# Optimization experiments

Hardware: AMD Instinct MI355X
Metric: run time of the kernel (lower is better)

The kernel has to match this reference:

```python
import jax, jax.numpy as jnp
import numpy as np

IN_F = 4096
OUT_F = 4096
BITS = 8
EPS = 1e-5
BATCH, SEQ = 4, 2048


def setup_inputs() -> dict:
    key = jax.random.key(0)
    k1, k2, k3 = jax.random.split(key, 3)
    bound = 1.0 / np.sqrt(IN_F)
    x = jax.random.normal(k1, (BATCH, SEQ, IN_F), dtype=jnp.float32)
    weight = jax.random.uniform(k2, (OUT_F, IN_F), dtype=jnp.float32, minval=-bound, maxval=bound)
    bias = jax.random.uniform(k3, (OUT_F,), dtype=jnp.float32, minval=-bound, maxval=bound)
    return {"x": x, "weight": weight, "bias": bias}


def _ste_round_clip(v, lo, hi):
    # round+clip with straight-through estimator
    q = jnp.clip(jnp.round(v), lo, hi)
    return v + jax.lax.stop_gradient(q - v)


def reference(x, weight, bias):
    q = jnp.float32(2 ** (BITS - 1))  # 128 for int8
    # weight ternarization: absmean scale, round to {-1,0,1}
    w_scale = jnp.maximum(jnp.mean(jnp.abs(weight)), EPS)
    w_q = _ste_round_clip(weight / w_scale, -1.0, 1.0)  # ternary [O,I]
    # activation int8 quantization: absmax scale over whole tensor (dim=None)
    gamma = jnp.maximum(jnp.max(jnp.abs(x)), EPS)
    x_q = _ste_round_clip(x * (q / gamma), -q, q - 1.0)  # int8 range values
    # integer-domain matmul then dequantize
    out = jnp.einsum('bsi,oi->bso', x_q, w_q) * (gamma * w_scale / q)
    return out + bias
```

## Files before the change

### kernel.cpp

```cpp
#include <hip/hip_runtime.h>
#include <stdint.h>

#define GLOBAL_AS __attribute__((address_space(1)))
#define LDS_AS __attribute__((address_space(3)))

typedef int v4i  __attribute__((ext_vector_type(4)));
typedef int v16i __attribute__((ext_vector_type(16)));

static constexpr int M = 8192;
static constexpr int N = 4096;
static constexpr int K = 4096;
static constexpr float F_EPS = 1e-5f;


__global__ void reduce_kernel(const float4* __restrict__ x, const float4* __restrict__ w,
                              float* __restrict__ pmax, double* __restrict__ psum) {
    const int b = blockIdx.x;
    const int t = threadIdx.x;
    if (b < 2048) {
        float m = 0.f;
        const int n4 = M * K / 4;
        int i = b * 512 + t;
        for (; i + 256 < n4; i += 2048 * 512) {
            float4 v0 = x[i];
            float4 v1 = x[i + 256];
            m = fmaxf(m, fmaxf(fmaxf(fabsf(v0.x), fabsf(v0.y)), fmaxf(fabsf(v0.z), fabsf(v0.w))));
            m = fmaxf(m, fmaxf(fmaxf(fabsf(v1.x), fabsf(v1.y)), fmaxf(fabsf(v1.z), fabsf(v1.w))));
        }
#pragma unroll
        for (int off = 32; off > 0; off >>= 1) m = fmaxf(m, __shfl_down(m, off, 64));
        __shared__ float red[4];
        if ((t & 63) == 0) red[t >> 6] = m;
        __syncthreads();
        if (t == 0) pmax[b] = fmaxf(fmaxf(red[0], red[1]), fmaxf(red[2], red[3]));
    } else {
        double s = 0.0;
        const int n4 = N * K / 4;
        int i = (b - 2048) * 512 + t;
        for (; i + 256 < n4; i += 1024 * 512) {
            float4 v0 = w[i];
            float4 v1 = w[i + 256];
            s += (double)fabsf(v0.x) + (double)fabsf(v0.y) + (double)fabsf(v0.z) + (double)fabsf(v0.w);
            s += (double)fabsf(v1.x) + (double)fabsf(v1.y) + (double)fabsf(v1.z) + (double)fabsf(v1.w);
        }
#pragma unroll
        for (int off = 32; off > 0; off >>= 1) s += __shfl_down(s, off, 64);
        __shared__ double dred[4];
        if ((t & 63) == 0) dred[t >> 6] = s;
        __syncthreads();
        if (t == 0) psum[b - 2048] = dred[0] + dred[1] + dred[2] + dred[3];
    }
}

__global__ void finalize_kernel(float* __restrict__ wssc, const float* __restrict__ pmax,
                                const double* __restrict__ psum) {
    const int t = threadIdx.x;
    float m = 0.f;
#pragma unroll
    for (int j = 0; j < 8; ++j) m = fmaxf(m, pmax[t + j * 256]);
#pragma unroll
    for (int off = 32; off > 0; off >>= 1) m = fmaxf(m, __shfl_down(m, off, 64));
    double s = psum[t] + psum[t + 256] + psum[t + 512] + psum[t + 768];
#pragma unroll
    for (int off = 32; off > 0; off >>= 1) s += __shfl_down(s, off, 64);
    __shared__ float red[4];
    __shared__ double dred[4];
    if ((t & 63) == 0) { red[t >> 6] = m; dred[t >> 6] = s; }
    __syncthreads();
    if (t == 0) {
        float gamma = fmaxf(fmaxf(fmaxf(red[0], red[1]), fmaxf(red[2], red[3])), F_EPS);
        double sum = dred[0] + dred[1] + dred[2] + dred[3];
        float wscale = (float)fmax(sum * (1.0 / ((double)N * (double)K)), (double)F_EPS);
        wssc[0] = 128.f / gamma;
        wssc[1] = wscale;
        wssc[2] = gamma * wscale / 128.f;
    }
}

__global__ void quant_kernel(const float4* __restrict__ x, const float4* __restrict__ w,
                             int* __restrict__ xq, int* __restrict__ wq,
                             const float* __restrict__ wssc) {
    const int b = blockIdx.x;
    const int t = threadIdx.x;
    if (b < 2048) {
        const float s = wssc[0];
        const int n4 = M * K / 4;
        int i = b * 512 + t;
        for (; i + 256 < n4; i += 2048 * 512) {
            float4 v0 = x[i];
            float4 v1 = x[i + 256];
            int a0 = min(127, max(-128, (int)rintf(v0.x * s)));
            int a1 = min(127, max(-128, (int)rintf(v0.y * s)));
            int a2 = min(127, max(-128, (int)rintf(v0.z * s)));
            int a3 = min(127, max(-128, (int)rintf(v0.w * s)));
            xq[i] = (a0 & 255) | ((a1 & 255) << 8) | ((a2 & 255) << 16) | (a3 << 24);
            int b0 = min(127, max(-128, (int)rintf(v1.x * s)));
            int b1 = min(127, max(-128, (int)rintf(v1.y * s)));
            int b2 = min(127, max(-128, (int)rintf(v1.z * s)));
            int b3 = min(127, max(-128, (int)rintf(v1.w * s)));
            xq[i + 256] = (b0 & 255) | ((b1 & 255) << 8) | ((b2 & 255) << 16) | (b3 << 24);
        }
    } else {
        const float ws = wssc[1];
        const int n4 = N * K / 4;
        int i = (b - 2048) * 512 + t;
        for (; i + 256 < n4; i += 1024 * 512) {
            float4 v0 = w[i];
            float4 v1 = w[i + 256];
            int a0 = min(1, max(-1, (int)rintf(v0.x / ws)));
            int a1 = min(1, max(-1, (int)rintf(v0.y / ws)));
            int a2 = min(1, max(-1, (int)rintf(v0.z / ws)));
            int a3 = min(1, max(-1, (int)rintf(v0.w / ws)));
            wq[i] = (a0 & 255) | ((a1 & 255) << 8) | ((a2 & 255) << 16) | (a3 << 24);
            int b0 = min(1, max(-1, (int)rintf(v1.x / ws)));
            int b1 = min(1, max(-1, (int)rintf(v1.y / ws)));
            int b2 = min(1, max(-1, (int)rintf(v1.z / ws)));
            int b3 = min(1, max(-1, (int)rintf(v1.w / ws)));
            wq[i + 256] = (b0 & 255) | ((b1 & 255) << 8) | ((b2 & 255) << 16) | (b3 << 24);
        }
    }
}

__global__ __launch_bounds__(512, 2) void gemm_kernel(
    const int8_t* __restrict__ xq, const int8_t* __restrict__ wq,
    const float* __restrict__ bias, const float* __restrict__ wssc,
    float* __restrict__ out) {

    __shared__ __align__(16) int8_t As[4][256 * 64];
    __shared__ __align__(16) int8_t Bs[4][256 * 64];

    const int t = threadIdx.x;
    const int lane = t & 63;
    const int wv = t >> 6;
    const int half = lane >> 5;
    const int lr = lane & 31;
    const int wm0 = (wv >> 2) * 128;
    const int wn0 = (wv & 3) * 64;

    const int bid = blockIdx.x;
    const int xcd = bid & 7;
    const int cix = bid >> 3;
    const int m0 = ((xcd >> 1) * 8 + (cix >> 3)) * 256;
    const int n0 = ((xcd & 1) * 8 + (cix & 7)) * 256;

    const GLOBAL_AS int8_t* aSrc[2];
    const GLOBAL_AS int8_t* bSrc[2];
    int aLds[2], bLds[2];
#pragma unroll
    for (int j = 0; j < 2; ++j) {
        int idx = j * 512 + t;
        int c = idx >> 6;
        int s = idx & 63;
        int k = s >> 4;
        int rho = ((s & 15) - 4 * k) & 15;
        int row = c * 16 + rho;
        aSrc[j] = (const GLOBAL_AS int8_t*)(xq + (size_t)(m0 + row) * K + k * 16);
        bSrc[j] = (const GLOBAL_AS int8_t*)(wq + (size_t)(n0 + row) * K + k * 16);
        aLds[j] = idx * 16;
        bLds[j] = idx * 16;
    }

    int aOff[2][4], bOff[2][2];
#pragma unroll
    for (int ks = 0; ks < 2; ++ks) {
        int k = ks * 2 + half;
#pragma unroll
        for (int q = 0; q < 4; ++q) {
            int r = wm0 + q * 32 + lr;
            aOff[ks][q] = (r >> 4) * 1024 + k * 256 + (((r & 15) + 4 * k) & 15) * 16;
        }
#pragma unroll
        for (int q = 0; q < 2; ++q) {
            int r = wn0 + q * 32 + lr;
            bOff[ks][q] = (r >> 4) * 1024 + k * 256 + (((r & 15) + 4 * k) & 15) * 16;
        }
    }

    v16i acc[4][2];
#pragma unroll
    for (int mt = 0; mt < 4; ++mt)
#pragma unroll
        for (int nt = 0; nt < 2; ++nt)
#pragma unroll
            for (int e = 0; e < 16; ++e) acc[mt][nt][e] = 0;

    auto stage = [&](int kt, int8_t* A, int8_t* B) {
#pragma unroll
        for (int j = 0; j < 2; ++j)
            __builtin_amdgcn_global_load_lds((const GLOBAL_AS void*)(aSrc[j] + kt),
                                             (LDS_AS void*)(A + aLds[j]), 16, 0, 0);
#pragma unroll
        for (int j = 0; j < 2; ++j)
            __builtin_amdgcn_global_load_lds((const GLOBAL_AS void*)(bSrc[j] + kt),
                                             (LDS_AS void*)(B + bLds[j]), 16, 0, 0);
    };

    auto compute = [&](const int8_t* A, const int8_t* B) {
#pragma unroll
        for (int ks = 0; ks < 2; ++ks) {
            v4i a[4], b[2];
#pragma unroll
            for (int q = 0; q < 4; ++q) a[q] = *(const v4i*)(A + aOff[ks][q]);
#pragma unroll
            for (int q = 0; q < 2; ++q) b[q] = *(const v4i*)(B + bOff[ks][q]);
            __builtin_amdgcn_s_setprio(1);
#pragma unroll
            for (int mt = 0; mt < 4; ++mt)
#pragma unroll
                for (int nt = 0; nt < 2; ++nt)
                    acc[mt][nt] = __builtin_amdgcn_mfma_i32_32x32x32_i8(a[mt], b[nt], acc[mt][nt], 0, 0, 0);
            __builtin_amdgcn_s_setprio(0);
        }
    };

#define FENCE() asm volatile("" ::: "memory")
#define PIPE_STEP(NB, CB, KT)                                        \
    do {                                                             \
        stage((KT) * 64, As[NB], Bs[NB]);                            \
        asm volatile("s_waitcnt vmcnt(12)" ::: "memory");            \
        __builtin_amdgcn_s_barrier();                                \
        FENCE();                                                     \
        compute(As[CB], Bs[CB]);                                     \
        FENCE();                                                     \
        __builtin_amdgcn_s_barrier();                                \
        FENCE();                                                     \
    } while (0)

    stage(0, As[0], Bs[0]);
    stage(64, As[1], Bs[1]);
    stage(128, As[2], Bs[2]);

#pragma unroll 1
    for (int tb = 0; tb < 56; tb += 4) {
        PIPE_STEP(3, 0, tb + 3);
        PIPE_STEP(0, 1, tb + 4);
        PIPE_STEP(1, 2, tb + 5);
        PIPE_STEP(2, 3, tb + 6);
    }
    PIPE_STEP(3, 0, 59);
    PIPE_STEP(0, 1, 60);
    PIPE_STEP(1, 2, 61);
    PIPE_STEP(2, 3, 62);
    PIPE_STEP(3, 0, 63);
    asm volatile("s_waitcnt vmcnt(8)" ::: "memory");
    __builtin_amdgcn_s_barrier(); FENCE();
    compute(As[1], Bs[1]); FENCE();
    __builtin_amdgcn_s_barrier(); FENCE();
    asm volatile("s_waitcnt vmcnt(4)" ::: "memory");
    __builtin_amdgcn_s_barrier(); FENCE();
    compute(As[2], Bs[2]); FENCE();
    __builtin_amdgcn_s_barrier(); FENCE();
    asm volatile("s_waitcnt vmcnt(0)" ::: "memory");
    __builtin_amdgcn_s_barrier(); FENCE();
    compute(As[3], Bs[3]);
#undef PIPE_STEP
#undef FENCE

    const float scale = wssc[2];
#pragma unroll
    for (int nt = 0; nt < 2; ++nt) {
        int col = n0 + wn0 + nt * 32 + lr;
        float bv = bias[col];
#pragma unroll
        for (int mt = 0; mt < 4; ++mt) {
            int rb = m0 + wm0 + mt * 32 + 4 * half;
#pragma unroll
            for (int reg = 0; reg < 16; ++reg) {
                int row = rb + (reg & 3) + 8 * (reg >> 2);
                out[(size_t)row * N + col] = (float)acc[mt][nt][reg] * scale + bv;
            }
        }
    }
}

extern "C" void kernel_launch(void* const* d_in, const int* in_sizes, int n_in,
                              void* d_out, int out_size, void* d_ws, size_t ws_size,
                              hipStream_t stream) {
    const float* x = (const float*)d_in[0];
    const float* w = (const float*)d_in[1];
    const float* bias = (const float*)d_in[2];
    float* out = (float*)d_out;

    float* wssc = (float*)d_ws;
    float* pmax = (float*)((char*)d_ws + 256);
    double* psum = (double*)((char*)d_ws + 8448);
    int8_t* xq = (int8_t*)d_ws + 16640;
    int8_t* wq = xq + (size_t)M * K;

    hipLaunchKernelGGL(reduce_kernel, dim3(3072), dim3(256), 0, stream,
                       (const float4*)x, (const float4*)w, pmax, psum);
    hipLaunchKernelGGL(finalize_kernel, dim3(1), dim3(256), 0, stream, wssc, pmax, psum);
    hipLaunchKernelGGL(quant_kernel, dim3(3072), dim3(256), 0, stream,
                       (const float4*)x, (const float4*)w, (int*)xq, (int*)wq, wssc);
    hipLaunchKernelGGL(gemm_kernel, dim3(M / 128 / 2 * N / 256 / 2 * 2), dim3(512), 0, stream,
                       xq, wq, bias, wssc, out);
}
```

Measured before the change: 459.7 us.

## Interleave staged A/B global loads with per-k-substep MFMA phases in int8 GEMM

Measured after the change: 497.8 us. +8.3%, slower.

```diff
diff --git a/kernel.cpp b/kernel.cpp
--- a/kernel.cpp
+++ b/kernel.cpp
@@ -184,77 +184,78 @@
 #pragma unroll
             for (int e = 0; e < 16; ++e) acc[mt][nt][e] = 0;
 
-    auto stage = [&](int kt, int8_t* A, int8_t* B) {
+    auto stageA = [&](int8_t* A, int kt) {
 #pragma unroll
         for (int j = 0; j < 2; ++j)
             __builtin_amdgcn_global_load_lds((const GLOBAL_AS void*)(aSrc[j] + kt),
                                              (LDS_AS void*)(A + aLds[j]), 16, 0, 0);
+    };
+    auto stageB = [&](int8_t* B, int kt) {
 #pragma unroll
         for (int j = 0; j < 2; ++j)
             __builtin_amdgcn_global_load_lds((const GLOBAL_AS void*)(bSrc[j] + kt),
                                              (LDS_AS void*)(B + bLds[j]), 16, 0, 0);
     };
 
-    auto compute = [&](const int8_t* A, const int8_t* B) {
-#pragma unroll
-        for (int ks = 0; ks < 2; ++ks) {
-            v4i a[4], b[2];
-#pragma unroll
-            for (int q = 0; q < 4; ++q) a[q] = *(const v4i*)(A + aOff[ks][q]);
-#pragma unroll
-            for (int q = 0; q < 2; ++q) b[q] = *(const v4i*)(B + bOff[ks][q]);
-            __builtin_amdgcn_s_setprio(1);
-#pragma unroll
-            for (int mt = 0; mt < 4; ++mt)
-#pragma unroll
-                for (int nt = 0; nt < 2; ++nt)
-                    acc[mt][nt] = __builtin_amdgcn_mfma_i32_32x32x32_i8(a[mt], b[nt], acc[mt][nt], 0, 0, 0);
-            __builtin_amdgcn_s_setprio(0);
-        }
-    };
-
-#define FENCE() asm volatile("" ::: "memory")
-#define PIPE_STEP(NB, CB, KT)                                        \
-    do {                                                             \
-        stage((KT) * 64, As[NB], Bs[NB]);                            \
-        asm volatile("s_waitcnt vmcnt(12)" ::: "memory");            \
-        __builtin_amdgcn_s_barrier();                                \
-        FENCE();                                                     \
-        compute(As[CB], Bs[CB]);                                     \
-        FENCE();                                                     \
-        __builtin_amdgcn_s_barrier();                                \
-        FENCE();                                                     \
+#define MFMA_I8(A_, B_, C_) __builtin_amdgcn_mfma_i32_32x32x32_i8(A_, B_, C_, 0, 0, 0)
+
+#define PHASE(Ab, Bb, KS, STAGEFN)                                          \
+    do {                                                                    \
+        v4i a0_ = *(const v4i*)((Ab) + aOff[KS][0]);                        \
+        v4i a1_ = *(const v4i*)((Ab) + aOff[KS][1]);                        \
+        v4i a2_ = *(const v4i*)((Ab) + aOff[KS][2]);                        \
+        v4i a3_ = *(const v4i*)((Ab) + aOff[KS][3]);                        \
+        v4i b0_ = *(const v4i*)((Bb) + bOff[KS][0]);                        \
+        v4i b1_ = *(const v4i*)((Bb) + bOff[KS][1]);                        \
+        STAGEFN;                                                            \
+        asm volatile("" ::: "memory");                                      \
+        __builtin_amdgcn_s_barrier();                                       \
+        __builtin_amdgcn_s_setprio(1);                                      \
+        acc[0][0] = MFMA_I8(a0_, b0_, acc[0][0]);                           \
+        acc[0][1] = MFMA_I8(a0_, b1_, acc[0][1]);                           \
+        acc[1][0] = MFMA_I8(a1_, b0_, acc[1][0]);                           \
+        acc[1][1] = MFMA_I8(a1_, b1_, acc[1][1]);                           \
+        acc[2][0] = MFMA_I8(a2_, b0_, acc[2][0]);                           \
+        acc[2][1] = MFMA_I8(a2_, b1_, acc[2][1]);                           \
+        acc[3][0] = MFMA_I8(a3_, b0_, acc[3][0]);                           \
+        acc[3][1] = MFMA_I8(a3_, b1_, acc[3][1]);                           \
+        __builtin_amdgcn_s_setprio(0);                                      \
+        asm volatile("" ::: "memory");                                      \
     } while (0)
 
-    stage(0, As[0], Bs[0]);
-    stage(64, As[1], Bs[1]);
-    stage(128, As[2], Bs[2]);
+#define TILE_END(VM)                                                        \
+    do {                                                                    \
+        asm volatile("s_waitcnt vmcnt(" #VM ")" ::: "memory");              \
+        __builtin_amdgcn_s_barrier();                                       \
+    } while (0)
+
+    stageA(As[0], 0);   stageB(Bs[0], 0);
+    stageA(As[1], 64);  stageB(Bs[1], 64);
+    stageA(As[2], 128); stageB(Bs[2], 128);
+    TILE_END(8);
 
 #pragma unroll 1
-    for (int tb = 0; tb < 56; tb += 4) {
-        PIPE_STEP(3, 0, tb + 3);
-        PIPE_STEP(0, 1, tb + 4);
-        PIPE_STEP(1, 2, tb + 5);
-        PIPE_STEP(2, 3, tb + 6);
-    }
-    PIPE_STEP(3, 0, 59);
-    PIPE_STEP(0, 1, 60);
-    PIPE_STEP(1, 2, 61);
-    PIPE_STEP(2, 3, 62);
-    PIPE_STEP(3, 0, 63);
-    asm volatile("s_waitcnt vmcnt(8)" ::: "memory");
-    __builtin_amdgcn_s_barrier(); FENCE();
-    compute(As[1], Bs[1]); FENCE();
-    __builtin_amdgcn_s_barrier(); FENCE();
-    asm volatile("s_waitcnt vmcnt(4)" ::: "memory");
-    __builtin_amdgcn_s_barrier(); FENCE();
-    compute(As[2], Bs[2]); FENCE();
-    __builtin_amdgcn_s_barrier(); FENCE();
-    asm volatile("s_waitcnt vmcnt(0)" ::: "memory");
-    __builtin_amdgcn_s_barrier(); FENCE();
-    compute(As[3], Bs[3]);
-#undef PIPE_STEP
-#undef FENCE
+    for (int tt = 0; tt < 61; ++tt) {
+        const int8_t* Ab = As[tt & 3];
+        const int8_t* Bb = Bs[tt & 3];
+        int8_t* An = As[(tt + 3) & 3];
+        int8_t* Bn = Bs[(tt + 3) & 3];
+        const int kt = (tt + 3) * 64;
+        PHASE(Ab, Bb, 0, stageA(An, kt));
+        PHASE(Ab, Bb, 1, stageB(Bn, kt));
+        TILE_END(8);
+    }
+    PHASE(As[61 & 3], Bs[61 & 3], 0, ((void)0));
+    PHASE(As[61 & 3], Bs[61 & 3], 1, ((void)0));
+    TILE_END(4);
+    PHASE(As[62 & 3], Bs[62 & 3], 0, ((void)0));
+    PHASE(As[62 & 3], Bs[62 & 3], 1, ((void)0));
+    TILE_END(0);
+    PHASE(As[63 & 3], Bs[63 & 3], 0, ((void)0));
+    PHASE(As[63 & 3], Bs[63 & 3], 1, ((void)0));
+#undef PHASE
+#undef TILE_END
+#undef MFMA_I8
 
     const float scale = wssc[2];
 #pragma unroll
@@ -292,6 +293,6 @@
     hipLaunchKernelGGL(finalize_kernel, dim3(1), dim3(256), 0, stream, wssc, pmax, psum);
     hipLaunchKernelGGL(quant_kernel, dim3(3072), dim3(256), 0, stream,
                        (const float4*)x, (const float4*)w, (int*)xq, (int*)wq, wssc);
-    hipLaunchKernelGGL(gemm_kernel, dim3(M / 128 / 2 * N / 256 / 2 * 2), dim3(512), 0, stream,
+    hipLaunchKernelGGL(gemm_kernel, dim3((M / 256) * (N / 256)), dim3(512), 0, stream,
                        xq, wq, bias, wssc, out);
 }
```

## Use 1024-thread blocks with smaller per-wave tiles and a double-buffered loop

Applied to the files above, without the earlier changes.

After: 487.8 us. 6.1% more time.

```diff
diff --git a/kernel.cpp b/kernel.cpp
--- a/kernel.cpp
+++ b/kernel.cpp
@@ -121,20 +121,20 @@
     }
 }
 
-__global__ __launch_bounds__(512, 2) void gemm_kernel(
+__global__ __launch_bounds__(1024, 3) void gemm_kernel(
     const int8_t* __restrict__ xq, const int8_t* __restrict__ wq,
     const float* __restrict__ bias, const float* __restrict__ wssc,
     float* __restrict__ out) {
 
-    __shared__ __align__(16) int8_t As[4][256 * 64];
-    __shared__ __align__(16) int8_t Bs[4][256 * 64];
+    __shared__ __align__(16) int8_t As[2][256 * 64];
+    __shared__ __align__(16) int8_t Bs[2][256 * 64];
 
     const int t = threadIdx.x;
     const int lane = t & 63;
     const int wv = t >> 6;
     const int half = lane >> 5;
     const int lr = lane & 31;
-    const int wm0 = (wv >> 2) * 128;
+    const int wm0 = (wv >> 2) * 64;
     const int wn0 = (wv & 3) * 64;
 
     const int bid = blockIdx.x;
@@ -143,69 +143,61 @@
     const int m0 = ((xcd >> 1) * 8 + (cix >> 3)) * 256;
     const int n0 = ((xcd & 1) * 8 + (cix & 7)) * 256;
 
-    const GLOBAL_AS int8_t* aSrc[2];
-    const GLOBAL_AS int8_t* bSrc[2];
-    int aLds[2], bLds[2];
-#pragma unroll
-    for (int j = 0; j < 2; ++j) {
-        int idx = j * 512 + t;
+    const GLOBAL_AS int8_t* aSrc;
+    const GLOBAL_AS int8_t* bSrc;
+    int ldsOff;
+    {
+        int idx = t;
         int c = idx >> 6;
         int s = idx & 63;
         int k = s >> 4;
         int rho = ((s & 15) - 4 * k) & 15;
         int row = c * 16 + rho;
-        aSrc[j] = (const GLOBAL_AS int8_t*)(xq + (size_t)(m0 + row) * K + k * 16);
-        bSrc[j] = (const GLOBAL_AS int8_t*)(wq + (size_t)(n0 + row) * K + k * 16);
-        aLds[j] = idx * 16;
-        bLds[j] = idx * 16;
-    }
-
-    int aOff[2][4], bOff[2][2];
+        aSrc = (const GLOBAL_AS int8_t*)(xq + (size_t)(m0 + row) * K + k * 16);
+        bSrc = (const GLOBAL_AS int8_t*)(wq + (size_t)(n0 + row) * K + k * 16);
+        ldsOff = idx * 16;
+    }
+
+    int aOff[2][2], bOff[2][2];
 #pragma unroll
     for (int ks = 0; ks < 2; ++ks) {
         int k = ks * 2 + half;
 #pragma unroll
-        for (int q = 0; q < 4; ++q) {
-            int r = wm0 + q * 32 + lr;
-            aOff[ks][q] = (r >> 4) * 1024 + k * 256 + (((r & 15) + 4 * k) & 15) * 16;
-        }
-#pragma unroll
         for (int q = 0; q < 2; ++q) {
-            int r = wn0 + q * 32 + lr;
-            bOff[ks][q] = (r >> 4) * 1024 + k * 256 + (((r & 15) + 4 * k) & 15) * 16;
-        }
-    }
-
-    v16i acc[4][2];
-#pragma unroll
-    for (int mt = 0; mt < 4; ++mt)
+            int ra = wm0 + q * 32 + lr;
+            aOff[ks][q] = (ra >> 4) * 1024 + k * 256 + (((ra & 15) + 4 * k) & 15) * 16;
+            int rb = wn0 + q * 32 + lr;
+            bOff[ks][q] = (rb >> 4) * 1024 + k * 256 + (((rb & 15) + 4 * k) & 15) * 16;
+        }
+    }
+
+    v16i acc[2][2];
+#pragma unroll
+    for (int mt = 0; mt < 2; ++mt)
 #pragma unroll
         for (int nt = 0; nt < 2; ++nt)
 #pragma unroll
             for (int e = 0; e < 16; ++e) acc[mt][nt][e] = 0;
 
     auto stage = [&](int kt, int8_t* A, int8_t* B) {
-#pragma unroll
-        for (int j = 0; j < 2; ++j)
-            __builtin_amdgcn_global_load_lds((const GLOBAL_AS void*)(aSrc[j] + kt),
-                                             (LDS_AS void*)(A + aLds[j]), 16, 0, 0);
-#pragma unroll
-        for (int j = 0; j < 2; ++j)
-            __builtin_amdgcn_global_load_lds((const GLOBAL_AS void*)(bSrc[j] + kt),
-                                             (LDS_AS void*)(B + bLds[j]), 16, 0, 0);
+        __builtin_amdgcn_global_load_lds((const GLOBAL_AS void*)(aSrc + kt),
+                                         (LDS_AS void*)(A + ldsOff), 16, 0, 0);
+        __builtin_amdgcn_global_load_lds((const GLOBAL_AS void*)(bSrc + kt),
+                                         (LDS_AS void*)(B + ldsOff), 16, 0, 0);
     };
 
     auto compute = [&](const int8_t* A, const int8_t* B) {
 #pragma unroll
         for (int ks = 0; ks < 2; ++ks) {
-            v4i a[4], b[2];
-#pragma unroll
-            for (int q = 0; q < 4; ++q) a[q] = *(const v4i*)(A + aOff[ks][q]);
-#pragma unroll
-            for (int q = 0; q < 2; ++q) b[q] = *(const v4i*)(B + bOff[ks][q]);
+            v4i a[2], b[2];
+#pragma unroll
+            for (int q = 0; q < 2; ++q) {
+                a[q] = *(const v4i*)(A + aOff[ks][q]);
+                b[q] = *(const v4i*)(B + bOff[ks][q]);
+            }
             __builtin_amdgcn_s_setprio(1);
 #pragma unroll
-            for (int mt = 0; mt < 4; ++mt)
+            for (int mt = 0; mt < 2; ++mt)
 #pragma unroll
                 for (int nt = 0; nt < 2; ++nt)
                     acc[mt][nt] = __builtin_amdgcn_mfma_i32_32x32x32_i8(a[mt], b[nt], acc[mt][nt], 0, 0, 0);
@@ -213,48 +205,16 @@
         }
     };
 
-#define FENCE() asm volatile("" ::: "memory")
-#define PIPE_STEP(NB, CB, KT)                                        \
-    do {                                                             \
-        stage((KT) * 64, As[NB], Bs[NB]);                            \
-        asm volatile("s_waitcnt vmcnt(12)" ::: "memory");            \
-        __builtin_amdgcn_s_barrier();                                \
-        FENCE();                                                     \
-        compute(As[CB], Bs[CB]);                                     \
-        FENCE();                                                     \
-        __builtin_amdgcn_s_barrier();                                \
-        FENCE();                                                     \
-    } while (0)
-
+    constexpr int NIT = K / 64;
     stage(0, As[0], Bs[0]);
-    stage(64, As[1], Bs[1]);
-    stage(128, As[2], Bs[2]);
-
+    __syncthreads();
 #pragma unroll 1
-    for (int tb = 0; tb < 56; tb += 4) {
-        PIPE_STEP(3, 0, tb + 3);
-        PIPE_STEP(0, 1, tb + 4);
-        PIPE_STEP(1, 2, tb + 5);
-        PIPE_STEP(2, 3, tb + 6);
-    }
-    PIPE_STEP(3, 0, 59);
-    PIPE_STEP(0, 1, 60);
-    PIPE_STEP(1, 2, 61);
-    PIPE_STEP(2, 3, 62);
-    PIPE_STEP(3, 0, 63);
-    asm volatile("s_waitcnt vmcnt(8)" ::: "memory");
-    __builtin_amdgcn_s_barrier(); FENCE();
-    compute(As[1], Bs[1]); FENCE();
-    __builtin_amdgcn_s_barrier(); FENCE();
-    asm volatile("s_waitcnt vmcnt(4)" ::: "memory");
-    __builtin_amdgcn_s_barrier(); FENCE();
-    compute(As[2], Bs[2]); FENCE();
-    __builtin_amdgcn_s_barrier(); FENCE();
-    asm volatile("s_waitcnt vmcnt(0)" ::: "memory");
-    __builtin_amdgcn_s_barrier(); FENCE();
-    compute(As[3], Bs[3]);
-#undef PIPE_STEP
-#undef FENCE
+    for (int tt = 0; tt < NIT - 1; ++tt) {
+        stage((tt + 1) * 64, As[(tt + 1) & 1], Bs[(tt + 1) & 1]);
+        compute(As[tt & 1], Bs[tt & 1]);
+        __syncthreads();
+    }
+    compute(As[(NIT - 1) & 1], Bs[(NIT - 1) & 1]);
 
     const float scale = wssc[2];
 #pragma unroll
@@ -262,7 +222,7 @@
         int col = n0 + wn0 + nt * 32 + lr;
         float bv = bias[col];
 #pragma unroll
-        for (int mt = 0; mt < 4; ++mt) {
+        for (int mt = 0; mt < 2; ++mt) {
             int rb = m0 + wm0 + mt * 32 + 4 * half;
 #pragma unroll
             for (int reg = 0; reg < 16; ++reg) {
@@ -292,6 +252,6 @@
     hipLaunchKernelGGL(finalize_kernel, dim3(1), dim3(256), 0, stream, wssc, pmax, psum);
     hipLaunchKernelGGL(quant_kernel, dim3(3072), dim3(256), 0, stream,
                        (const float4*)x, (const float4*)w, (int*)xq, (int*)wq, wssc);
-    hipLaunchKernelGGL(gemm_kernel, dim3(M / 128 / 2 * N / 256 / 2 * 2), dim3(512), 0, stream,
+    hipLaunchKernelGGL(gemm_kernel, dim3((M / 256) * (N / 256)), dim3(1024), 0, stream,
                        xq, wq, bias, wssc, out);
 }
```
